# Kernel optimization log

Hardware: AMD Instinct MI355X
Metric: run time of the kernel (lower is better)

The kernel has to match this reference:

```python
import jax, jax.numpy as jnp
import numpy as np

K = 5               # kernel size of the causal/dilated convs
N_LAYERS = 30       # params.n_dilation_conv_layers
CYCLE = 10          # n_dilation_conv_layers / n_dilation_cycles
MU = 255.0          # quantization_channels - 1 for mu-law expansion
B, T = 8, 262144


def dil_causal_conv(x, w, b, d):
    """Single-channel dilated causal conv. x:[B,1,T], w:[K], b:scalar/[1]."""
    P = (K - 1) * d
    xp = jnp.pad(x, ((0, 0), (0, 0), (P, 0)))
    Tn = x.shape[-1]
    # cross-correlation, matching torch Conv1d with left pad then right crop
    y = w[0] * xp[..., 0:Tn]
    for j in range(1, K):
        y = y + w[j] * xp[..., j * d: j * d + Tn]
    return y + b


def setup_inputs() -> dict:
    key = jax.random.key(0)
    ks = jax.random.split(key, 14)
    n = lambda k, shape, s=0.2: jax.random.normal(k, shape, dtype=jnp.float32) * s
    return {
        "x": jax.random.normal(ks[0], (B, 1, T), dtype=jnp.float32),
        "causal_w": n(ks[1], (K,)),
        "causal_b": n(ks[2], (1,)),
        "filter_w": n(ks[3], (N_LAYERS, K)),
        "filter_b": n(ks[4], (N_LAYERS,)),
        "gate_w": n(ks[5], (N_LAYERS, K)),
        "gate_b": n(ks[6], (N_LAYERS,)),
        "res_w": n(ks[7], (N_LAYERS,)),
        "res_b": n(ks[8], (N_LAYERS,)),
        "conv1_w": n(ks[9], (1,)),
        "conv1_b": n(ks[10], (1,)),
        "conv2_w": n(ks[11], (1,)),
        "conv2_b": n(ks[12], (1,)),
    }


def reference(x, causal_w, causal_b, filter_w, filter_b, gate_w, gate_b,
              res_w, res_b, conv1_w, conv1_b, conv2_w, conv2_b):
    dilations = [2 ** (k % CYCLE) for k in range(N_LAYERS)]
    h = dil_causal_conv(x, causal_w, causal_b, 1)
    skip = jnp.zeros_like(h)
    for k, d in enumerate(dilations):
        f = jnp.tanh(dil_causal_conv(h, filter_w[k], filter_b[k], d))
        g = jax.nn.sigmoid(dil_causal_conv(h, gate_w[k], gate_b[k], d))
        o = f * g                      # gated activation (skip output)
        h = res_w[k] * o + res_b[k] + h  # 1x1 residual conv + residual add
        skip = skip + o
    out = conv1_w * jax.nn.relu(skip) + conv1_b   # 1x1 conv
    out = conv2_w * jax.nn.relu(out) + conv2_b    # 1x1 conv
    # mu-law expanding, quantization_channels=256
    out = jnp.sign(out) * jnp.expm1(jnp.abs(out) * jnp.log1p(MU)) / MU
    return jax.nn.softmax(out, axis=-1)
```

## Files before the change

kernel.cpp:

```cpp
#include <hip/hip_runtime.h>

#define T_LEN 262144
#define B_SZ 8
#define CHUNK 8192
#define HALO 4096
#define NTHREADS 1024
#define NGROUPS ((CHUNK + HALO) / 4)
#define CHUNKS_PER_ROW (T_LEN / CHUNK)
#define NBLOCKS (B_SZ * CHUNKS_PER_ROW)
#define LOG2E 1.4426950408889634f
#define NEG2LOG2E (-2.8853900817779268f)
#define NEGLOG2E  (-1.4426950408889634f)

typedef float f32x2 __attribute__((ext_vector_type(2)));
typedef float f32x4 __attribute__((ext_vector_type(4)));

__device__ __forceinline__ float frcp(float x)  { return __builtin_amdgcn_rcpf(x); }
__device__ __forceinline__ float fexp2(float x) { return __builtin_amdgcn_exp2f(x); }
__device__ __forceinline__ f32x4 splat(float s) { f32x4 r = {s, s, s, s}; return r; }
__device__ __forceinline__ f32x2 pair(float s)  { f32x2 r = {s, s}; return r; }
__device__ __forceinline__ f32x2 lo2(f32x4 v)   { return __builtin_shufflevector(v, v, 0, 1); }
__device__ __forceinline__ f32x2 hi2(f32x4 v)   { return __builtin_shufflevector(v, v, 2, 3); }
__device__ __forceinline__ f32x4 cat4(f32x2 a, f32x2 b) {
    f32x4 r; r.x = a.x; r.y = a.y; r.z = b.x; r.w = b.y; return r;
}

__device__ __forceinline__ f32x2 pkfma2(f32x2 a, f32x2 b, f32x2 c) {
    f32x2 d;
    asm("v_pk_fma_f32 %0, %1, %2, %3" : "=v"(d) : "v"(a), "v"(b), "v"(c));
    return d;
}
__device__ __forceinline__ f32x2 pkadd2(f32x2 a, f32x2 b) {
    f32x2 d;
    asm("v_pk_add_f32 %0, %1, %2" : "=v"(d) : "v"(a), "v"(b));
    return d;
}
__device__ __forceinline__ f32x2 pksub2(f32x2 a, f32x2 b) {
    f32x2 d;
    asm("v_pk_add_f32 %0, %1, %2 neg_lo:[0,1] neg_hi:[0,1]" : "=v"(d) : "v"(a), "v"(b));
    return d;
}
__device__ __forceinline__ f32x2 pkmul2(f32x2 a, f32x2 b) {
    f32x2 d;
    asm("v_pk_mul_f32 %0, %1, %2" : "=v"(d) : "v"(a), "v"(b));
    return d;
}
__device__ __forceinline__ f32x4 pfma_s(f32x2 w, f32x4 v, f32x4 a) {
    return cat4(pkfma2(w, lo2(v), lo2(a)), pkfma2(w, hi2(v), hi2(a)));
}
__device__ __forceinline__ f32x4 pfma_v(f32x4 a, f32x4 b, f32x4 c) {
    return cat4(pkfma2(lo2(a), lo2(b), lo2(c)), pkfma2(hi2(a), hi2(b), hi2(c)));
}
__device__ __forceinline__ f32x4 padd_s(f32x2 s, f32x4 b) {
    return cat4(pkadd2(s, lo2(b)), pkadd2(s, hi2(b)));
}
__device__ __forceinline__ f32x4 padd_v(f32x4 a, f32x4 b) {
    return cat4(pkadd2(lo2(a), lo2(b)), pkadd2(hi2(a), hi2(b)));
}
__device__ __forceinline__ f32x4 psub_s(f32x2 s, f32x4 b) {
    return cat4(pksub2(s, lo2(b)), pksub2(s, hi2(b)));
}
__device__ __forceinline__ f32x4 pmul_v(f32x4 a, f32x4 b) {
    return cat4(pkmul2(lo2(a), lo2(b)), pkmul2(hi2(a), hi2(b)));
}

__device__ __forceinline__ uint2 pk4(f32x4 v) {
    uint2 u;
    u.x = __builtin_amdgcn_perm(__float_as_uint(v.y), __float_as_uint(v.x), 0x07060302u);
    u.y = __builtin_amdgcn_perm(__float_as_uint(v.w), __float_as_uint(v.z), 0x07060302u);
    return u;
}
__device__ __forceinline__ f32x4 up4(uint2 u) {
    f32x4 r;
    r.x = __uint_as_float(u.x << 16);
    r.y = __uint_as_float(u.x);
    r.z = __uint_as_float(u.y << 16);
    r.w = __uint_as_float(u.y);
    return r;
}
__device__ __forceinline__ f32x4 gate4(f32x4 af, f32x4 ag, f32x2 one) {
    f32x4 E1, E2, rc;
    E1.x = fexp2(af.x); E1.y = fexp2(af.y); E1.z = fexp2(af.z); E1.w = fexp2(af.w);
    E2.x = fexp2(ag.x); E2.y = fexp2(ag.y); E2.z = fexp2(ag.z); E2.w = fexp2(ag.w);
    f32x4 d1  = padd_s(one, E1);
    f32x4 den = pfma_v(E2, d1, d1);
    f32x4 num = psub_s(one, E1);
    rc.x = frcp(den.x); rc.y = frcp(den.y); rc.z = frcp(den.z); rc.w = frcp(den.w);
    return pmul_v(num, rc);
}
__device__ __forceinline__ float mulaw(float v, float c1wv, float c1bv, float c2wv, float c2bv) {
    float a  = __builtin_fmaf(c1wv, fmaxf(v, 0.0f), c1bv);
    float b2 = __builtin_fmaf(c2wv, fmaxf(a, 0.0f), c2bv);
    float m  = fexp2(fabsf(b2) * 8.0f) - 1.0f;
    return copysignf(m * (1.0f / 255.0f), b2);
}

template <int STAGE>
__global__ __launch_bounds__(NTHREADS, 4)
void stage_kernel(const void* __restrict__ in_,
                  const float* __restrict__ cw, const float* __restrict__ cb,
                  const float* __restrict__ fw, const float* __restrict__ fb,
                  const float* __restrict__ gw, const float* __restrict__ gb,
                  const float* __restrict__ rw, const float* __restrict__ rb,
                  uint2* __restrict__ hout, float* __restrict__ skio,
                  const float* __restrict__ c1w, const float* __restrict__ c1b,
                  const float* __restrict__ c2w, const float* __restrict__ c2b,
                  float2* __restrict__ blockstats)
{
    __shared__ uint2 bufl[2][NGROUPS];
    __shared__ float red[NTHREADS / 64];

    const int tid = threadIdx.x;
    const int bid = blockIdx.x;
    const int row = bid / CHUNKS_PER_ROW;
    const int chunk = bid % CHUNKS_PER_ROW;
    const int rowbase = row * T_LEN;
    const int base_t = chunk * CHUNK;
    const bool first = (chunk == 0);

    f32x4 h[3];
    if (STAGE == 0) {
        const float* inb = (const float*)in_ + rowbase + base_t - HALO;
        #pragma unroll
        for (int w = 0; w < 3; ++w) {
            int G = tid + w * NTHREADS;
            if (w == 0 && first) h[w] = splat(0.0f);
            else                 h[w] = *(const f32x4*)(inb + 4 * G);
            bufl[0][G] = pk4(h[w]);
        }
    } else {
        const uint2* inb = (const uint2*)in_ + ((rowbase + base_t - HALO) >> 2);
        #pragma unroll
        for (int w = 0; w < 3; ++w) {
            int G = tid + w * NTHREADS;
            uint2 u = (w == 0 && first) ? make_uint2(0u, 0u) : inb[G];
            bufl[0][G] = u;
            h[w] = up4(u);
        }
    }
    f32x4 sk[2];
    if (STAGE == 0) { sk[0] = splat(0.0f); sk[1] = splat(0.0f); }
    else {
        sk[0] = *(const f32x4*)(skio + rowbase + base_t + 4 * tid);
        sk[1] = *(const f32x4*)(skio + rowbase + base_t + 4096 + 4 * tid);
    }
    __syncthreads();

    const f32x2 ONE = pair(1.0f);

    if (STAGE == 0) {
        f32x2 CW[5];
        #pragma unroll
        for (int j = 0; j < 5; ++j) CW[j] = pair(cw[4 - j]);
        const f32x4 BB = splat(cb[0]);
        #pragma unroll
        for (int w = 0; w < 3; ++w) {
            int G = tid + w * NTHREADS;
            int gm = G - 1; if (w == 0) gm = gm < 0 ? 0 : gm;
            f32x4 T = up4(bufl[0][gm]);
            f32x4 hw = h[w];
            f32x4 t1 = __builtin_shufflevector(T, hw, 3, 4, 5, 6);
            f32x4 t2 = __builtin_shufflevector(T, hw, 2, 3, 4, 5);
            f32x4 t3 = __builtin_shufflevector(T, hw, 1, 2, 3, 4);
            f32x4 acc = pfma_s(CW[0], hw, BB);
            acc = pfma_s(CW[1], t1, acc);
            acc = pfma_s(CW[2], t2, acc);
            acc = pfma_s(CW[3], t3, acc);
            acc = pfma_s(CW[4], T, acc);
            if (w == 0 && first) acc = splat(0.0f);
            h[w] = acc;
            bufl[1][G] = pk4(acc);
        }
        __syncthreads();
    }

    #pragma unroll
    for (int k = 0; k < 10; ++k) {
        const int c = (STAGE == 0) ? ((k + 1) & 1) : (k & 1);
        const int d = 1 << k;
        const int L = STAGE * 10 + k;
        const float* fwL = fw + 5 * L;
        const float* gwL = gw + 5 * L;
        f32x2 WF[5], WG[5];
        #pragma unroll
        for (int j = 0; j < 5; ++j) {
            WF[j] = pair(fwL[4 - j] * NEG2LOG2E);
            WG[j] = pair(gwL[4 - j] * NEGLOG2E);
        }
        const f32x4 FB = splat(fb[L] * NEG2LOG2E), GB = splat(gb[L] * NEGLOG2E);
        const f32x2 RW = pair(rw[L]), RB = pair(rb[L]);
        const uint2* __restrict__ bufc = bufl[c];
        uint2* __restrict__ bufd = bufl[c ^ 1];

        #pragma unroll
        for (int w = 0; w < 3; ++w) {
            const int G = tid + w * NTHREADS;
            if (w == 0 && tid < (2 << k)) continue;
            f32x4 hw = h[w];
            f32x4 t1, t2, t3, t4;
            if (d >= 4) {
                const int DG = d >> 2;
                const uint2* bp = bufc + (G - 4 * DG);
                t4 = up4(bp[0]);
                t3 = up4(bp[DG]);
                t2 = up4(bp[2 * DG]);
                t1 = up4(bp[3 * DG]);
            } else if (d == 1) {
                f32x4 T = up4(bufc[G - 1]);
                t1 = __builtin_shufflevector(T, hw, 3, 4, 5, 6);
                t2 = __builtin_shufflevector(T, hw, 2, 3, 4, 5);
                t3 = __builtin_shufflevector(T, hw, 1, 2, 3, 4);
                t4 = T;
            } else {
                const uint2* bp = bufc + (G - 2);
                f32x4 T2 = up4(bp[0]);
                f32x4 T1 = up4(bp[1]);
                t1 = __builtin_shufflevector(T1, hw, 2, 3, 4, 5);
                t2 = T1;
                t3 = __builtin_shufflevector(T2, T1, 2, 3, 4, 5);
                t4 = T2;
            }
            f32x4 af = pfma_s(WF[0], hw, FB);
            af = pfma_s(WF[1], t1, af); af = pfma_s(WF[2], t2, af);
            af = pfma_s(WF[3], t3, af); af = pfma_s(WF[4], t4, af);
            f32x4 ag = pfma_s(WG[0], hw, GB);
            ag = pfma_s(WG[1], t1, ag); ag = pfma_s(WG[2], t2, ag);
            ag = pfma_s(WG[3], t3, ag); ag = pfma_s(WG[4], t4, ag);
            f32x4 o = gate4(af, ag, ONE);
            f32x4 nh = pfma_s(RW, o, padd_s(RB, hw));
            if (w == 0 && first) nh = splat(0.0f);
            h[w] = nh;
            if (k < 9) bufd[G] = pk4(nh);
            if (w == 1) sk[0] = padd_v(sk[0], o);
            if (w == 2) sk[1] = padd_v(sk[1], o);
        }
        if (k < 9) __syncthreads();
    }

    if (STAGE < 2) {
        uint2* hp = hout + ((rowbase + base_t) >> 2);
        hp[tid]        = pk4(h[1]);
        hp[tid + 1024] = pk4(h[2]);
        *(f32x4*)(skio + rowbase + base_t + 4 * tid)        = sk[0];
        *(f32x4*)(skio + rowbase + base_t + 4096 + 4 * tid) = sk[1];
    } else {
        const float c1wv = c1w[0], c1bv = c1b[0], c2wv = c2w[0], c2bv = c2b[0];
        f32x4 p1, p2;
        p1.x = mulaw(sk[0].x, c1wv, c1bv, c2wv, c2bv);
        p1.y = mulaw(sk[0].y, c1wv, c1bv, c2wv, c2bv);
        p1.z = mulaw(sk[0].z, c1wv, c1bv, c2wv, c2bv);
        p1.w = mulaw(sk[0].w, c1wv, c1bv, c2wv, c2bv);
        p2.x = mulaw(sk[1].x, c1wv, c1bv, c2wv, c2bv);
        p2.y = mulaw(sk[1].y, c1wv, c1bv, c2wv, c2bv);
        p2.z = mulaw(sk[1].z, c1wv, c1bv, c2wv, c2bv);
        p2.w = mulaw(sk[1].w, c1wv, c1bv, c2wv, c2bv);
        *(f32x4*)(skio + rowbase + base_t + 4 * tid)        = p1;
        *(f32x4*)(skio + rowbase + base_t + 4096 + 4 * tid) = p2;

        float pmax = fmaxf(fmaxf(fmaxf(p1.x, p1.y), fmaxf(p1.z, p1.w)),
                           fmaxf(fmaxf(p2.x, p2.y), fmaxf(p2.z, p2.w)));
        #pragma unroll
        for (int off = 32; off; off >>= 1) pmax = fmaxf(pmax, __shfl_xor(pmax, off, 64));
        if ((tid & 63) == 0) red[tid >> 6] = pmax;
        __syncthreads();
        float bmax = red[0];
        #pragma unroll
        for (int i = 1; i < NTHREADS / 64; ++i) bmax = fmaxf(bmax, red[i]);
        __syncthreads();

        float ps = fexp2((p1.x - bmax) * LOG2E) + fexp2((p1.y - bmax) * LOG2E)
                 + fexp2((p1.z - bmax) * LOG2E) + fexp2((p1.w - bmax) * LOG2E)
                 + fexp2((p2.x - bmax) * LOG2E) + fexp2((p2.y - bmax) * LOG2E)
                 + fexp2((p2.z - bmax) * LOG2E) + fexp2((p2.w - bmax) * LOG2E);
        #pragma unroll
        for (int off = 32; off; off >>= 1) ps += __shfl_xor(ps, off, 64);
        if ((tid & 63) == 0) red[tid >> 6] = ps;
        __syncthreads();
        if (tid == 0) {
            float s = 0.0f;
            #pragma unroll
            for (int i = 0; i < NTHREADS / 64; ++i) s += red[i];
            blockstats[bid] = make_float2(bmax, s);
        }
    }
}

__global__ __launch_bounds__(64)
void combine_kernel(const float2* __restrict__ bs, float2* __restrict__ rs)
{
    const int row = blockIdx.x;
    const int lane = threadIdx.x;
    float bm = -3.0e38f, s = 0.0f;
    if (lane < CHUNKS_PER_ROW) {
        float2 v = bs[row * CHUNKS_PER_ROW + lane];
        bm = v.x; s = v.y;
    }
    float m = bm;
    #pragma unroll
    for (int off = 32; off; off >>= 1) m = fmaxf(m, __shfl_xor(m, off, 64));
    float cc = s * fexp2((bm - m) * LOG2E);
    #pragma unroll
    for (int off = 32; off; off >>= 1) cc += __shfl_xor(cc, off, 64);
    if (lane == 0) rs[row] = make_float2(m, 1.0f / cc);
}

__global__ __launch_bounds__(NTHREADS)
void norm_kernel(float* __restrict__ p, const float2* __restrict__ rs)
{
    const int tid = threadIdx.x, bid = blockIdx.x;
    const int row = bid / CHUNKS_PER_ROW;
    const float2 st = rs[row];
    const int base = row * T_LEN + (bid % CHUNKS_PER_ROW) * CHUNK + 4 * tid;
    #pragma unroll
    for (int part = 0; part < 2; ++part) {
        float* q = p + base + part * 4096;
        f32x4 v = *(const f32x4*)q;
        v.x = fexp2((v.x - st.x) * LOG2E) * st.y;
        v.y = fexp2((v.y - st.x) * LOG2E) * st.y;
        v.z = fexp2((v.z - st.x) * LOG2E) * st.y;
        v.w = fexp2((v.w - st.x) * LOG2E) * st.y;
        *(f32x4*)q = v;
    }
}

extern "C" void kernel_launch(void* const* d_in, const int* in_sizes, int n_in,
                              void* d_out, int out_size, void* d_ws, size_t ws_size,
                              hipStream_t stream)
{
    (void)in_sizes; (void)n_in; (void)out_size; (void)ws_size;
    const float* x   = (const float*)d_in[0];
    const float* cw  = (const float*)d_in[1];
    const float* cb  = (const float*)d_in[2];
    const float* fw  = (const float*)d_in[3];
    const float* fb  = (const float*)d_in[4];
    const float* gw  = (const float*)d_in[5];
    const float* gb  = (const float*)d_in[6];
    const float* rw  = (const float*)d_in[7];
    const float* rb  = (const float*)d_in[8];
    const float* c1w = (const float*)d_in[9];
    const float* c1b = (const float*)d_in[10];
    const float* c2w = (const float*)d_in[11];
    const float* c2b = (const float*)d_in[12];
    float* out = (float*)d_out;

    const size_t NTOT = (size_t)B_SZ * T_LEN;
    uint2*  hA = (uint2*)d_ws;
    uint2*  hB = (uint2*)((char*)d_ws + NTOT * 2);
    float2* bs = (float2*)((char*)d_ws + NTOT * 4);
    float2* rs = (float2*)((char*)d_ws + NTOT * 4 + 8192);

    stage_kernel<0><<<NBLOCKS, NTHREADS, 0, stream>>>(x,  cw, cb, fw, fb, gw, gb, rw, rb,
                                                      hA, out, c1w, c1b, c2w, c2b, bs);
    stage_kernel<1><<<NBLOCKS, NTHREADS, 0, stream>>>(hA, cw, cb, fw, fb, gw, gb, rw, rb,
                                                      hB, out, c1w, c1b, c2w, c2b, bs);
    stage_kernel<2><<<NBLOCKS, NTHREADS, 0, stream>>>(hB, cw, cb, fw, fb, gw, gb, rw, rb,
                                                      nullptr, out, c1w, c1b, c2w, c2b, bs);
    combine_kernel<<<B_SZ, 64, 0, stream>>>(bs, rs);
    norm_kernel<<<NBLOCKS, NTHREADS, 0, stream>>>(out, rs);
}
```

Before: 78.51 us.

## Switch conv accumulation and residual/skip state from bf16/fp32 to packed fp16

Result: no change. 77.42 us (-1.4%).

```diff
diff --git a/kernel.cpp b/kernel.cpp
--- a/kernel.cpp
+++ b/kernel.cpp
@@ -14,16 +14,30 @@
 
 typedef float f32x2 __attribute__((ext_vector_type(2)));
 typedef float f32x4 __attribute__((ext_vector_type(4)));
+typedef _Float16 f16x2 __attribute__((ext_vector_type(2)));
+typedef __fp16 fp16x2 __attribute__((ext_vector_type(2)));
 
 __device__ __forceinline__ float frcp(float x)  { return __builtin_amdgcn_rcpf(x); }
 __device__ __forceinline__ float fexp2(float x) { return __builtin_amdgcn_exp2f(x); }
-__device__ __forceinline__ f32x4 splat(float s) { f32x4 r = {s, s, s, s}; return r; }
 __device__ __forceinline__ f32x2 pair(float s)  { f32x2 r = {s, s}; return r; }
 __device__ __forceinline__ f32x2 lo2(f32x4 v)   { return __builtin_shufflevector(v, v, 0, 1); }
 __device__ __forceinline__ f32x2 hi2(f32x4 v)   { return __builtin_shufflevector(v, v, 2, 3); }
 __device__ __forceinline__ f32x4 cat4(f32x2 a, f32x2 b) {
     f32x4 r; r.x = a.x; r.y = a.y; r.z = b.x; r.w = b.y; return r;
 }
+__device__ __forceinline__ unsigned b32(f16x2 v) { return __builtin_bit_cast(unsigned, v); }
+__device__ __forceinline__ f16x2 hbits(unsigned u) { return __builtin_bit_cast(f16x2, u); }
+__device__ __forceinline__ f16x2 hsplat(float s) { _Float16 h = (_Float16)s; f16x2 r = {h, h}; return r; }
+__device__ __forceinline__ f16x2 hfma(f16x2 a, f16x2 b, f16x2 c) { return __builtin_elementwise_fma(a, b, c); }
+__device__ __forceinline__ f16x2 pkrtz(float x, float y) {
+    fp16x2 t = __builtin_amdgcn_cvt_pkrtz(x, y);
+    return __builtin_bit_cast(f16x2, t);
+}
+__device__ __forceinline__ f32x4 h2f4(f16x2 a, f16x2 b) {
+    f32x2 lo = __builtin_convertvector(a, f32x2);
+    f32x2 hi = __builtin_convertvector(b, f32x2);
+    return cat4(lo, hi);
+}
 
 __device__ __forceinline__ f32x2 pkfma2(f32x2 a, f32x2 b, f32x2 c) {
     f32x2 d;
@@ -45,18 +59,12 @@
     asm("v_pk_mul_f32 %0, %1, %2" : "=v"(d) : "v"(a), "v"(b));
     return d;
 }
-__device__ __forceinline__ f32x4 pfma_s(f32x2 w, f32x4 v, f32x4 a) {
-    return cat4(pkfma2(w, lo2(v), lo2(a)), pkfma2(w, hi2(v), hi2(a)));
-}
 __device__ __forceinline__ f32x4 pfma_v(f32x4 a, f32x4 b, f32x4 c) {
     return cat4(pkfma2(lo2(a), lo2(b), lo2(c)), pkfma2(hi2(a), hi2(b), hi2(c)));
 }
 __device__ __forceinline__ f32x4 padd_s(f32x2 s, f32x4 b) {
     return cat4(pkadd2(s, lo2(b)), pkadd2(s, hi2(b)));
 }
-__device__ __forceinline__ f32x4 padd_v(f32x4 a, f32x4 b) {
-    return cat4(pkadd2(lo2(a), lo2(b)), pkadd2(hi2(a), hi2(b)));
-}
 __device__ __forceinline__ f32x4 psub_s(f32x2 s, f32x4 b) {
     return cat4(pksub2(s, lo2(b)), pksub2(s, hi2(b)));
 }
@@ -64,20 +72,6 @@
     return cat4(pkmul2(lo2(a), lo2(b)), pkmul2(hi2(a), hi2(b)));
 }
 
-__device__ __forceinline__ uint2 pk4(f32x4 v) {
-    uint2 u;
-    u.x = __builtin_amdgcn_perm(__float_as_uint(v.y), __float_as_uint(v.x), 0x07060302u);
-    u.y = __builtin_amdgcn_perm(__float_as_uint(v.w), __float_as_uint(v.z), 0x07060302u);
-    return u;
-}
-__device__ __forceinline__ f32x4 up4(uint2 u) {
-    f32x4 r;
-    r.x = __uint_as_float(u.x << 16);
-    r.y = __uint_as_float(u.x);
-    r.z = __uint_as_float(u.y << 16);
-    r.w = __uint_as_float(u.y);
-    return r;
-}
 __device__ __forceinline__ f32x4 gate4(f32x4 af, f32x4 ag, f32x2 one) {
     f32x4 E1, E2, rc;
     E1.x = fexp2(af.x); E1.y = fexp2(af.y); E1.z = fexp2(af.z); E1.w = fexp2(af.w);
@@ -102,7 +96,8 @@
                   const float* __restrict__ fw, const float* __restrict__ fb,
                   const float* __restrict__ gw, const float* __restrict__ gb,
                   const float* __restrict__ rw, const float* __restrict__ rb,
-                  uint2* __restrict__ hout, float* __restrict__ skio,
+                  uint2* __restrict__ hout, uint2* __restrict__ skbuf,
+                  float* __restrict__ pout,
                   const float* __restrict__ c1w, const float* __restrict__ c1b,
                   const float* __restrict__ c2w, const float* __restrict__ c2b,
                   float2* __restrict__ blockstats)
@@ -117,16 +112,21 @@
     const int rowbase = row * T_LEN;
     const int base_t = chunk * CHUNK;
     const bool first = (chunk == 0);
-
-    f32x4 h[3];
+    const f16x2 HZ = hsplat(0.0f);
+
+    f16x2 hA[3], hB[3];
     if (STAGE == 0) {
         const float* inb = (const float*)in_ + rowbase + base_t - HALO;
         #pragma unroll
         for (int w = 0; w < 3; ++w) {
             int G = tid + w * NTHREADS;
-            if (w == 0 && first) h[w] = splat(0.0f);
-            else                 h[w] = *(const f32x4*)(inb + 4 * G);
-            bufl[0][G] = pk4(h[w]);
+            if (w == 0 && first) { hA[w] = HZ; hB[w] = HZ; }
+            else {
+                f32x4 v = *(const f32x4*)(inb + 4 * G);
+                hA[w] = pkrtz(v.x, v.y);
+                hB[w] = pkrtz(v.z, v.w);
+            }
+            bufl[0][G] = make_uint2(b32(hA[w]), b32(hB[w]));
         }
     } else {
         const uint2* inb = (const uint2*)in_ + ((rowbase + base_t - HALO) >> 2);
@@ -135,41 +135,42 @@
             int G = tid + w * NTHREADS;
             uint2 u = (w == 0 && first) ? make_uint2(0u, 0u) : inb[G];
             bufl[0][G] = u;
-            h[w] = up4(u);
-        }
-    }
-    f32x4 sk[2];
-    if (STAGE == 0) { sk[0] = splat(0.0f); sk[1] = splat(0.0f); }
+            hA[w] = hbits(u.x); hB[w] = hbits(u.y);
+        }
+    }
+    f16x2 s1A, s1B, s2A, s2B;
+    const int skb = ((rowbase + base_t) >> 2) + tid;
+    if (STAGE == 0) { s1A = HZ; s1B = HZ; s2A = HZ; s2B = HZ; }
     else {
-        sk[0] = *(const f32x4*)(skio + rowbase + base_t + 4 * tid);
-        sk[1] = *(const f32x4*)(skio + rowbase + base_t + 4096 + 4 * tid);
+        uint2 u1 = skbuf[skb], u2 = skbuf[skb + 1024];
+        s1A = hbits(u1.x); s1B = hbits(u1.y);
+        s2A = hbits(u2.x); s2B = hbits(u2.y);
     }
     __syncthreads();
 
     const f32x2 ONE = pair(1.0f);
 
     if (STAGE == 0) {
-        f32x2 CW[5];
-        #pragma unroll
-        for (int j = 0; j < 5; ++j) CW[j] = pair(cw[4 - j]);
-        const f32x4 BB = splat(cb[0]);
+        const f16x2 C0 = hsplat(cw[4]), C1 = hsplat(cw[3]), C2 = hsplat(cw[2]),
+                    C3 = hsplat(cw[1]), C4 = hsplat(cw[0]), BB = hsplat(cb[0]);
         #pragma unroll
         for (int w = 0; w < 3; ++w) {
             int G = tid + w * NTHREADS;
             int gm = G - 1; if (w == 0) gm = gm < 0 ? 0 : gm;
-            f32x4 T = up4(bufl[0][gm]);
-            f32x4 hw = h[w];
-            f32x4 t1 = __builtin_shufflevector(T, hw, 3, 4, 5, 6);
-            f32x4 t2 = __builtin_shufflevector(T, hw, 2, 3, 4, 5);
-            f32x4 t3 = __builtin_shufflevector(T, hw, 1, 2, 3, 4);
-            f32x4 acc = pfma_s(CW[0], hw, BB);
-            acc = pfma_s(CW[1], t1, acc);
-            acc = pfma_s(CW[2], t2, acc);
-            acc = pfma_s(CW[3], t3, acc);
-            acc = pfma_s(CW[4], T, acc);
-            if (w == 0 && first) acc = splat(0.0f);
-            h[w] = acc;
-            bufl[1][G] = pk4(acc);
+            uint2 P = bufl[0][gm];
+            unsigned uA = b32(hA[w]), uB = b32(hB[w]);
+            unsigned t1A = __builtin_amdgcn_perm(uA, P.y, 0x05040302u);
+            unsigned t1B = __builtin_amdgcn_perm(uB, uA, 0x05040302u);
+            unsigned t3A = __builtin_amdgcn_perm(P.y, P.x, 0x05040302u);
+            f16x2 aA = hfma(C0, hA[w], BB);
+            f16x2 aB = hfma(C0, hB[w], BB);
+            aA = hfma(C1, hbits(t1A), aA); aB = hfma(C1, hbits(t1B), aB);
+            aA = hfma(C2, hbits(P.y), aA); aB = hfma(C2, hbits(uA), aB);
+            aA = hfma(C3, hbits(t3A), aA); aB = hfma(C3, hbits(t1A), aB);
+            aA = hfma(C4, hbits(P.x), aA); aB = hfma(C4, hbits(P.y), aB);
+            if (w == 0 && first) { aA = HZ; aB = HZ; }
+            hA[w] = aA; hB[w] = aB;
+            bufl[1][G] = make_uint2(b32(aA), b32(aB));
         }
         __syncthreads();
     }
@@ -181,14 +182,14 @@
         const int L = STAGE * 10 + k;
         const float* fwL = fw + 5 * L;
         const float* gwL = gw + 5 * L;
-        f32x2 WF[5], WG[5];
-        #pragma unroll
-        for (int j = 0; j < 5; ++j) {
-            WF[j] = pair(fwL[4 - j] * NEG2LOG2E);
-            WG[j] = pair(gwL[4 - j] * NEGLOG2E);
-        }
-        const f32x4 FB = splat(fb[L] * NEG2LOG2E), GB = splat(gb[L] * NEGLOG2E);
-        const f32x2 RW = pair(rw[L]), RB = pair(rb[L]);
+        const f16x2 WF0 = hsplat(fwL[4] * NEG2LOG2E), WF1 = hsplat(fwL[3] * NEG2LOG2E),
+                    WF2 = hsplat(fwL[2] * NEG2LOG2E), WF3 = hsplat(fwL[1] * NEG2LOG2E),
+                    WF4 = hsplat(fwL[0] * NEG2LOG2E);
+        const f16x2 WG0 = hsplat(gwL[4] * NEGLOG2E), WG1 = hsplat(gwL[3] * NEGLOG2E),
+                    WG2 = hsplat(gwL[2] * NEGLOG2E), WG3 = hsplat(gwL[1] * NEGLOG2E),
+                    WG4 = hsplat(gwL[0] * NEGLOG2E);
+        const f16x2 FB = hsplat(fb[L] * NEG2LOG2E), GB = hsplat(gb[L] * NEGLOG2E);
+        const f16x2 RW = hsplat(rw[L]), RB = hsplat(rb[L]);
         const uint2* __restrict__ bufc = bufl[c];
         uint2* __restrict__ bufd = bufl[c ^ 1];
 
@@ -196,66 +197,76 @@
         for (int w = 0; w < 3; ++w) {
             const int G = tid + w * NTHREADS;
             if (w == 0 && tid < (2 << k)) continue;
-            f32x4 hw = h[w];
-            f32x4 t1, t2, t3, t4;
+            f16x2 cA = hA[w], cB = hB[w];
+            f16x2 t1a, t1b, t2a, t2b, t3a, t3b, t4a, t4b;
             if (d >= 4) {
                 const int DG = d >> 2;
                 const uint2* bp = bufc + (G - 4 * DG);
-                t4 = up4(bp[0]);
-                t3 = up4(bp[DG]);
-                t2 = up4(bp[2 * DG]);
-                t1 = up4(bp[3 * DG]);
+                uint2 U4 = bp[0], U3 = bp[DG], U2 = bp[2 * DG], U1 = bp[3 * DG];
+                t1a = hbits(U1.x); t1b = hbits(U1.y);
+                t2a = hbits(U2.x); t2b = hbits(U2.y);
+                t3a = hbits(U3.x); t3b = hbits(U3.y);
+                t4a = hbits(U4.x); t4b = hbits(U4.y);
             } else if (d == 1) {
-                f32x4 T = up4(bufc[G - 1]);
-                t1 = __builtin_shufflevector(T, hw, 3, 4, 5, 6);
-                t2 = __builtin_shufflevector(T, hw, 2, 3, 4, 5);
-                t3 = __builtin_shufflevector(T, hw, 1, 2, 3, 4);
-                t4 = T;
+                uint2 P = bufc[G - 1];
+                unsigned uA = b32(cA);
+                unsigned w1A = __builtin_amdgcn_perm(uA, P.y, 0x05040302u);
+                unsigned w1B = __builtin_amdgcn_perm(b32(cB), uA, 0x05040302u);
+                unsigned w3A = __builtin_amdgcn_perm(P.y, P.x, 0x05040302u);
+                t1a = hbits(w1A); t1b = hbits(w1B);
+                t2a = hbits(P.y); t2b = cA;
+                t3a = hbits(w3A); t3b = hbits(w1A);
+                t4a = hbits(P.x); t4b = hbits(P.y);
             } else {
-                const uint2* bp = bufc + (G - 2);
-                f32x4 T2 = up4(bp[0]);
-                f32x4 T1 = up4(bp[1]);
-                t1 = __builtin_shufflevector(T1, hw, 2, 3, 4, 5);
-                t2 = T1;
-                t3 = __builtin_shufflevector(T2, T1, 2, 3, 4, 5);
-                t4 = T2;
+                uint2 P = bufc[G - 1], Q = bufc[G - 2];
+                t1a = hbits(P.y); t1b = cA;
+                t2a = hbits(P.x); t2b = hbits(P.y);
+                t3a = hbits(Q.y); t3b = hbits(P.x);
+                t4a = hbits(Q.x); t4b = hbits(Q.y);
             }
-            f32x4 af = pfma_s(WF[0], hw, FB);
-            af = pfma_s(WF[1], t1, af); af = pfma_s(WF[2], t2, af);
-            af = pfma_s(WF[3], t3, af); af = pfma_s(WF[4], t4, af);
-            f32x4 ag = pfma_s(WG[0], hw, GB);
-            ag = pfma_s(WG[1], t1, ag); ag = pfma_s(WG[2], t2, ag);
-            ag = pfma_s(WG[3], t3, ag); ag = pfma_s(WG[4], t4, ag);
-            f32x4 o = gate4(af, ag, ONE);
-            f32x4 nh = pfma_s(RW, o, padd_s(RB, hw));
-            if (w == 0 && first) nh = splat(0.0f);
-            h[w] = nh;
-            if (k < 9) bufd[G] = pk4(nh);
-            if (w == 1) sk[0] = padd_v(sk[0], o);
-            if (w == 2) sk[1] = padd_v(sk[1], o);
+            f16x2 afA = hfma(WF0, cA, FB), afB = hfma(WF0, cB, FB);
+            afA = hfma(WF1, t1a, afA); afB = hfma(WF1, t1b, afB);
+            afA = hfma(WF2, t2a, afA); afB = hfma(WF2, t2b, afB);
+            afA = hfma(WF3, t3a, afA); afB = hfma(WF3, t3b, afB);
+            afA = hfma(WF4, t4a, afA); afB = hfma(WF4, t4b, afB);
+            f16x2 agA = hfma(WG0, cA, GB), agB = hfma(WG0, cB, GB);
+            agA = hfma(WG1, t1a, agA); agB = hfma(WG1, t1b, agB);
+            agA = hfma(WG2, t2a, agA); agB = hfma(WG2, t2b, agB);
+            agA = hfma(WG3, t3a, agA); agB = hfma(WG3, t3b, agB);
+            agA = hfma(WG4, t4a, agA); agB = hfma(WG4, t4b, agB);
+            f32x4 o = gate4(h2f4(afA, afB), h2f4(agA, agB), ONE);
+            f16x2 oA = pkrtz(o.x, o.y), oB = pkrtz(o.z, o.w);
+            f16x2 nA = hfma(RW, oA, cA + RB);
+            f16x2 nB = hfma(RW, oB, cB + RB);
+            if (w == 0 && first) { nA = HZ; nB = HZ; }
+            hA[w] = nA; hB[w] = nB;
+            if (k < 9) bufd[G] = make_uint2(b32(nA), b32(nB));
+            if (w == 1) { s1A = s1A + oA; s1B = s1B + oB; }
+            if (w == 2) { s2A = s2A + oA; s2B = s2B + oB; }
         }
         if (k < 9) __syncthreads();
     }
 
     if (STAGE < 2) {
         uint2* hp = hout + ((rowbase + base_t) >> 2);
-        hp[tid]        = pk4(h[1]);
-        hp[tid + 1024] = pk4(h[2]);
-        *(f32x4*)(skio + rowbase + base_t + 4 * tid)        = sk[0];
-        *(f32x4*)(skio + rowbase + base_t + 4096 + 4 * tid) = sk[1];
+        hp[tid]        = make_uint2(b32(hA[1]), b32(hB[1]));
+        hp[tid + 1024] = make_uint2(b32(hA[2]), b32(hB[2]));
+        skbuf[skb]        = make_uint2(b32(s1A), b32(s1B));
+        skbuf[skb + 1024] = make_uint2(b32(s2A), b32(s2B));
     } else {
         const float c1wv = c1w[0], c1bv = c1b[0], c2wv = c2w[0], c2bv = c2b[0];
+        f32x4 sk1 = h2f4(s1A, s1B), sk2 = h2f4(s2A, s2B);
         f32x4 p1, p2;
-        p1.x = mulaw(sk[0].x, c1wv, c1bv, c2wv, c2bv);
-        p1.y = mulaw(sk[0].y, c1wv, c1bv, c2wv, c2bv);
-        p1.z = mulaw(sk[0].z, c1wv, c1bv, c2wv, c2bv);
-        p1.w = mulaw(sk[0].w, c1wv, c1bv, c2wv, c2bv);
-        p2.x = mulaw(sk[1].x, c1wv, c1bv, c2wv, c2bv);
-        p2.y = mulaw(sk[1].y, c1wv, c1bv, c2wv, c2bv);
-        p2.z = mulaw(sk[1].z, c1wv, c1bv, c2wv, c2bv);
-        p2.w = mulaw(sk[1].w, c1wv, c1bv, c2wv, c2bv);
-        *(f32x4*)(skio + rowbase + base_t + 4 * tid)        = p1;
-        *(f32x4*)(skio + rowbase + base_t + 4096 + 4 * tid) = p2;
+        p1.x = mulaw(sk1.x, c1wv, c1bv, c2wv, c2bv);
+        p1.y = mulaw(sk1.y, c1wv, c1bv, c2wv, c2bv);
+        p1.z = mulaw(sk1.z, c1wv, c1bv, c2wv, c2bv);
+        p1.w = mulaw(sk1.w, c1wv, c1bv, c2wv, c2bv);
+        p2.x = mulaw(sk2.x, c1wv, c1bv, c2wv, c2bv);
+        p2.y = mulaw(sk2.y, c1wv, c1bv, c2wv, c2bv);
+        p2.z = mulaw(sk2.z, c1wv, c1bv, c2wv, c2bv);
+        p2.w = mulaw(sk2.w, c1wv, c1bv, c2wv, c2bv);
+        *(f32x4*)(pout + rowbase + base_t + 4 * tid)        = p1;
+        *(f32x4*)(pout + rowbase + base_t + 4096 + 4 * tid) = p2;
 
         float pmax = fmaxf(fmaxf(fmaxf(p1.x, p1.y), fmaxf(p1.z, p1.w)),
                            fmaxf(fmaxf(p2.x, p2.y), fmaxf(p2.z, p2.w)));
@@ -345,16 +356,17 @@
 
     const size_t NTOT = (size_t)B_SZ * T_LEN;
     uint2*  hA = (uint2*)d_ws;
-    uint2*  hB = (uint2*)((char*)d_ws + NTOT * 2);
-    float2* bs = (float2*)((char*)d_ws + NTOT * 4);
-    float2* rs = (float2*)((char*)d_ws + NTOT * 4 + 8192);
+    uint2*  hB = (uint2*)((char*)d_ws + 2 * NTOT);
+    uint2*  sk = (uint2*)((char*)d_ws + 4 * NTOT);
+    float2* bs = (float2*)((char*)d_ws + 6 * NTOT);
+    float2* rs = (float2*)((char*)d_ws + 6 * NTOT + 8192);
 
     stage_kernel<0><<<NBLOCKS, NTHREADS, 0, stream>>>(x,  cw, cb, fw, fb, gw, gb, rw, rb,
-                                                      hA, out, c1w, c1b, c2w, c2b, bs);
+                                                      hA, sk, out, c1w, c1b, c2w, c2b, bs);
     stage_kernel<1><<<NBLOCKS, NTHREADS, 0, stream>>>(hA, cw, cb, fw, fb, gw, gb, rw, rb,
-                                                      hB, out, c1w, c1b, c2w, c2b, bs);
+                                                      hB, sk, out, c1w, c1b, c2w, c2b, bs);
     stage_kernel<2><<<NBLOCKS, NTHREADS, 0, stream>>>(hB, cw, cb, fw, fb, gw, gb, rw, rb,
-                                                      nullptr, out, c1w, c1b, c2w, c2b, bs);
+                                                      nullptr, sk, out, c1w, c1b, c2w, c2b, bs);
     combine_kernel<<<B_SZ, 64, 0, stream>>>(bs, rs);
     norm_kernel<<<NBLOCKS, NTHREADS, 0, stream>>>(out, rs);
 }
```
